# Kernel optimization log

Hardware: AMD Instinct MI355X
Metric: run time of the kernel (lower is better)

The kernel has to match this reference:

```python
import jax, jax.numpy as jnp
import numpy as np

TEMPERATURE = 0.1
NEG_INF = -9e15

def setup_inputs() -> dict:
    key = jax.random.key(0)
    k1, k2 = jax.random.split(key)
    B, D = 4096, 256
    z_i = jax.random.normal(k1, (B, D), dtype=jnp.float32)
    z_j = jax.random.normal(k2, (B, D), dtype=jnp.float32)
    return {"z_i": z_i, "z_j": z_j}

def _l2norm(x, eps=1e-12):
    # matches F.normalize(dim=1): x / max(||x||, eps)
    n = jnp.sqrt(jnp.sum(x * x, axis=1, keepdims=True))
    return x / jnp.maximum(n, eps)

def reference(z_i, z_j):
    B = z_i.shape[0]
    zi = _l2norm(z_i)
    zj = _l2norm(z_j)
    reps = jnp.concatenate([zi, zj], axis=0)  # [2B, D], unit rows
    # cosine similarity of unit vectors == dot product
    sim = reps @ reps.T  # [2B, 2B]
    N = 2 * B
    eye = jnp.eye(N, dtype=bool)
    sim = jnp.where(eye, NEG_INF, sim)
    # positives: offset +B and -B diagonals
    pos = jnp.concatenate([sim[jnp.arange(B), jnp.arange(B) + B],
                           sim[jnp.arange(B) + B, jnp.arange(B)]], axis=0)  # [2B]
    pos = pos / TEMPERATURE
    sim = sim / TEMPERATURE
    denom = jnp.sum(jnp.exp(sim), axis=1)  # [2B]
    loss = -jnp.mean(pos - jnp.log(denom))
    return loss
```

## Files before the change

kernel.cpp:

```cpp
#include <hip/hip_runtime.h>
#include <hip/hip_bf16.h>
#include <stdint.h>

#define NROWS 8192
#define BROWS 4096
#define LN2 0.6931471805599453f
#define FSC 8.944507e-4f
#define KMAD 7503
#define CBITS 1064989150
#define NBLK 2112

typedef __attribute__((ext_vector_type(4))) int i32x4;

__device__ inline void gload_lds16(const void* g, void* l) {
  __builtin_amdgcn_global_load_lds((const __attribute__((address_space(1))) void*)g,
                                   (__attribute__((address_space(3))) void*)l,
                                   16, 0, 0);
}

__global__ __launch_bounds__(256) void knorm(const float* __restrict__ zi,
                                             const float* __restrict__ zj,
                                             int* __restrict__ reps,
                                             int* __restrict__ qss,
                                             int* __restrict__ tab,
                                             float* __restrict__ denom,
                                             float* __restrict__ out) {
  int w = threadIdx.x >> 6, l = threadIdx.x & 63;
  int row = blockIdx.x * 4 + w;
  const float* src = (row < BROWS) ? (zi + (size_t)row * 256)
                                   : (zj + (size_t)(row - BROWS) * 256);
  float4 v = ((const float4*)src)[l];
  float ss = v.x * v.x + v.y * v.y + v.z * v.z + v.w * v.w;
#pragma unroll
  for (int m = 1; m < 64; m <<= 1) ss += __shfl_xor(ss, m, 64);
  float sc = 127.0f / fmaxf(sqrtf(ss), 1e-12f);
  int q0 = __float2int_rn(v.x * sc), q1 = __float2int_rn(v.y * sc);
  int q2 = __float2int_rn(v.z * sc), q3 = __float2int_rn(v.w * sc);
  reps[(size_t)row * 64 + l] =
      (q0 & 255) | ((q1 & 255) << 8) | ((q2 & 255) << 16) | ((q3 & 255) << 24);
  int qs = q0 * q0 + q1 * q1 + q2 * q2 + q3 * q3;
#pragma unroll
  for (int m = 1; m < 64; m <<= 1) qs += __shfl_xor(qs, m, 64);
  if (l == 0) { denom[row] = 0.f; qss[row] = qs; }
  if (row == 0 && l == 0) out[0] = 0.f;

  int gid = blockIdx.x * 256 + threadIdx.x;
  if (gid < NBLK) {
    int orig = (gid & 7) * 264 + (gid >> 3);
    int rem = orig, it = 0, ch;
    while (rem >= (ch = (128 - it + 3) >> 2)) { rem -= ch; ++it; }
    tab[gid] = it | (rem << 16);
  }
}

__global__ __launch_bounds__(64, 2) void ksim(const int* __restrict__ reps_,
                                              const int* __restrict__ tab,
                                              float* __restrict__ denom,
                                              float* __restrict__ pos) {
  __shared__ uint4 smem[2][512];
  int l = threadIdx.x;
  int kgrp = l >> 4;

  int v = tab[blockIdx.x];
  int it = v & 0xffff, q = v >> 16;
  int rowbase = it * 64;
  int cs0 = rowbase + q * 256;
  int len = NROWS - cs0; if (len > 256) len = 256;
  int ntile = len >> 5;

  auto stage = [&](int bufi, int colbase) {
#pragma unroll
    for (int i = 0; i < 8; ++i) {
      int lr = i * 4 + (l >> 4);
      int kb = ((l & 15) * 16) ^ ((lr & 15) << 4);
      gload_lds16((const char*)reps_ + (size_t)(colbase + lr) * 256 + kb,
                  (void*)&smem[bufi][i * 64]);
    }
  };
  stage(0, cs0);

  i32x4 a[4][4];
  {
    const uint4* r4 = (const uint4*)reps_;
    int arow = rowbase + (l & 15);
#pragma unroll
    for (int fr = 0; fr < 4; ++fr)
#pragma unroll
      for (int kk = 0; kk < 4; ++kk)
        a[fr][kk] = __builtin_bit_cast(i32x4,
            r4[(size_t)(arow + fr * 16) * 16 + kk * 4 + kgrp]);
  }

  float rowsum[4][4];
#pragma unroll
  for (int fr = 0; fr < 4; ++fr)
#pragma unroll
    for (int r = 0; r < 4; ++r) rowsum[fr][r] = 0.f;

  int r0 = rowbase + kgrp * 4;
  int buf = 0;
  const int kmad = KMAD;
  const int cbits = CBITS;

  for (int t = 0; t < ntile; ++t) {
    if (t + 1 < ntile) {
      stage(buf ^ 1, cs0 + 32 * (t + 1));
      asm volatile("s_waitcnt vmcnt(8)" ::: "memory");
    } else {
      asm volatile("s_waitcnt vmcnt(0)" ::: "memory");
    }
    __builtin_amdgcn_sched_barrier(0);

    const char* bb = (const char*)&smem[0][0] + buf * 8192;
    i32x4 acc[4][2];
    const i32x4 zero = {0, 0, 0, 0};
    __builtin_amdgcn_s_setprio(1);
#pragma unroll
    for (int kk = 0; kk < 4; ++kk) {
      i32x4 bf[2];
#pragma unroll
      for (int fc = 0; fc < 2; ++fc) {
        int lr = (l & 15) + fc * 16;
        bf[fc] = *(const i32x4*)(bb + lr * 256 + ((((kk * 4 + kgrp) ^ (lr & 15))) << 4));
      }
#pragma unroll
      for (int fr = 0; fr < 4; ++fr)
#pragma unroll
        for (int fc = 0; fc < 2; ++fc) {
          if (kk == 0)
            acc[fr][fc] = __builtin_amdgcn_mfma_i32_16x16x64_i8(a[fr][0], bf[fc], zero, 0, 0, 0);
          else
            acc[fr][fc] = __builtin_amdgcn_mfma_i32_16x16x64_i8(a[fr][kk], bf[fc], acc[fr][fc], 0, 0, 0);
        }
    }
    __builtin_amdgcn_s_setprio(0);

    int cb = cs0 + 32 * t;
    bool docol = !(q == 0 && t < 2);
    bool dopos = (q == 16) && (t < 2);
    float cp0 = 0.f, cp1 = 0.f;
#pragma unroll
    for (int fr = 0; fr < 4; ++fr)
#pragma unroll
      for (int fc = 0; fc < 2; ++fc)
#pragma unroll
        for (int r = 0; r < 4; ++r) {
          int I = acc[fr][fc][r];
          int ib;
          asm("v_mad_i32_i24 %0, %1, %2, %3"
              : "=v"(ib) : "v"(I), "s"(kmad), "v"(cbits));
          float e = __builtin_bit_cast(float, ib);
          if (dopos) {
            int rg = r0 + fr * 16 + r;
            int cg = cb + (l & 15) + fc * 16;
            if (cg == rg + BROWS) pos[rg] = (float)I * FSC;
          }
          rowsum[fr][r] += e;
          if (fc == 0) cp0 += e; else cp1 += e;
        }
    if (docol) {
      cp0 += __shfl_xor(cp0, 16, 64); cp0 += __shfl_xor(cp0, 32, 64);
      cp1 += __shfl_xor(cp1, 16, 64); cp1 += __shfl_xor(cp1, 32, 64);
      if (l < 16) {
        atomicAdd(&denom[cb + l], cp0);
        atomicAdd(&denom[cb + 16 + l], cp1);
      }
    }
    buf ^= 1;
  }

#pragma unroll
  for (int fr = 0; fr < 4; ++fr)
#pragma unroll
    for (int r = 0; r < 4; ++r) {
      float vv = rowsum[fr][r];
      vv += __shfl_xor(vv, 1, 64);
      vv += __shfl_xor(vv, 2, 64);
      vv += __shfl_xor(vv, 4, 64);
      vv += __shfl_xor(vv, 8, 64);
      if ((l & 15) == 0) atomicAdd(&denom[r0 + fr * 16 + r], vv);
    }
}

__global__ __launch_bounds__(256) void kfin(const float* __restrict__ denom,
                                            const float* __restrict__ pos,
                                            const int* __restrict__ qss,
                                            float* __restrict__ out) {
  int i = blockIdx.x * 256 + threadIdx.x;
  int ib = qss[i] * KMAD + CBITS;
  float diag_e = __builtin_bit_cast(float, ib);
  float v = (logf(denom[i] - diag_e) - pos[i & 4095] * LN2) * (1.0f / 8192.0f);
#pragma unroll
  for (int m = 1; m < 64; m <<= 1) v += __shfl_xor(v, m, 64);
  __shared__ float part[4];
  if ((threadIdx.x & 63) == 0) part[threadIdx.x >> 6] = v;
  __syncthreads();
  if (threadIdx.x == 0)
    atomicAdd(out, part[0] + part[1] + part[2] + part[3]);
}

extern "C" void kernel_launch(void* const* d_in, const int* in_sizes, int n_in,
                              void* d_out, int out_size, void* d_ws, size_t ws_size,
                              hipStream_t stream) {
  (void)in_sizes; (void)n_in; (void)out_size; (void)ws_size;
  const float* zi = (const float*)d_in[0];
  const float* zj = (const float*)d_in[1];
  float* out = (float*)d_out;
  char* ws = (char*)d_ws;
  int* reps    = (int*)ws;
  float* denom = (float*)(ws + 2097152);
  float* pos   = (float*)(ws + 2097152 + 32768);
  int* qss     = (int*)(ws + 2097152 + 32768 + 16384);
  int* tab     = (int*)(ws + 2097152 + 32768 + 16384 + 32768);

  knorm<<<2048, 256, 0, stream>>>(zi, zj, reps, qss, tab, denom, out);
  ksim<<<NBLK, 64, 0, stream>>>(reps, tab, denom, pos);
  kfin<<<32, 256, 0, stream>>>(denom, pos, qss, out);
}
```

Before: 40.62 us.

## Triple-buffer column tiles and defer column-sum atomics to block end

Moves the LDS staging of B tiles from double to triple buffering, prefetching two tiles ahead with adjusted vmcnt waits so global loads overlap more compute. Column partial sums are kept in a shared-memory array instead of being atomically added to global denom each tile, and are flushed once at the end of the block, skipping zero entries. This trades extra LDS use (about 24KB plus 1KB), which may lower occupancy, for fewer global atomics and deeper latency hiding.

```diff
diff --git a/kernel.cpp b/kernel.cpp
--- a/kernel.cpp
+++ b/kernel.cpp
@@ -57,7 +57,8 @@
                                               const int* __restrict__ tab,
                                               float* __restrict__ denom,
                                               float* __restrict__ pos) {
-  __shared__ uint4 smem[2][512];
+  __shared__ uint4 smem[3][512];
+  __shared__ float colacc[256];
   int l = threadIdx.x;
   int kgrp = l >> 4;
 
@@ -68,13 +69,16 @@
   int len = NROWS - cs0; if (len > 256) len = 256;
   int ntile = len >> 5;
 
-  auto stage = [&](int bufi, int colbase) {
+  colacc[l] = 0.f; colacc[l + 64] = 0.f;
+  colacc[l + 128] = 0.f; colacc[l + 192] = 0.f;
+
+  auto stage = [&](int slot, int colbase) {
 #pragma unroll
     for (int i = 0; i < 8; ++i) {
       int lr = i * 4 + (l >> 4);
       int kb = ((l & 15) * 16) ^ ((lr & 15) << 4);
       gload_lds16((const char*)reps_ + (size_t)(colbase + lr) * 256 + kb,
-                  (void*)&smem[bufi][i * 64]);
+                  (void*)&smem[slot][i * 64]);
     }
   };
   stage(0, cs0);
@@ -90,6 +94,7 @@
         a[fr][kk] = __builtin_bit_cast(i32x4,
             r4[(size_t)(arow + fr * 16) * 16 + kk * 4 + kgrp]);
   }
+  if (ntile > 1) stage(1, cs0 + 32);
 
   float rowsum[4][4];
 #pragma unroll
@@ -98,20 +103,23 @@
     for (int r = 0; r < 4; ++r) rowsum[fr][r] = 0.f;
 
   int r0 = rowbase + kgrp * 4;
-  int buf = 0;
+  int slot = 0;
   const int kmad = KMAD;
   const int cbits = CBITS;
 
   for (int t = 0; t < ntile; ++t) {
-    if (t + 1 < ntile) {
-      stage(buf ^ 1, cs0 + 32 * (t + 1));
+    if (t + 2 < ntile) {
+      int ns = slot + 2; if (ns >= 3) ns -= 3;
+      stage(ns, cs0 + 32 * (t + 2));
+      asm volatile("s_waitcnt vmcnt(16)" ::: "memory");
+    } else if (t + 1 < ntile) {
       asm volatile("s_waitcnt vmcnt(8)" ::: "memory");
     } else {
       asm volatile("s_waitcnt vmcnt(0)" ::: "memory");
     }
     __builtin_amdgcn_sched_barrier(0);
 
-    const char* bb = (const char*)&smem[0][0] + buf * 8192;
+    const char* bb = (const char*)&smem[0][0] + slot * 8192;
     i32x4 acc[4][2];
     const i32x4 zero = {0, 0, 0, 0};
     __builtin_amdgcn_s_setprio(1);
@@ -162,11 +170,12 @@
       cp0 += __shfl_xor(cp0, 16, 64); cp0 += __shfl_xor(cp0, 32, 64);
       cp1 += __shfl_xor(cp1, 16, 64); cp1 += __shfl_xor(cp1, 32, 64);
       if (l < 16) {
-        atomicAdd(&denom[cb + l], cp0);
-        atomicAdd(&denom[cb + 16 + l], cp1);
+        int off = (cb - cs0) + l;
+        colacc[off] += cp0;
+        colacc[off + 16] += cp1;
       }
     }
-    buf ^= 1;
+    ++slot; if (slot >= 3) slot = 0;
   }
 
 #pragma unroll
@@ -180,6 +189,13 @@
       vv += __shfl_xor(vv, 8, 64);
       if ((l & 15) == 0) atomicAdd(&denom[r0 + fr * 16 + r], vv);
     }
+
+#pragma unroll
+  for (int i = 0; i < 4; ++i) {
+    int off = l + 64 * i;
+    float vv = colacc[off];
+    if (vv != 0.f) atomicAdd(&denom[cs0 + off], vv);
+  }
 }
 
 __global__ __launch_bounds__(256) void kfin(const float* __restrict__ denom,
```

New measurement: 54.02 us. +33.0%, slower.
